# Optimization experiments

Measured on AMD Instinct MI355X. Metric: run time of the kernel, lower is better.

The kernel has to match this reference:

```python
import jax, jax.numpy as jnp
import numpy as np

EPS = 1e-5  # BatchNorm eps; eval mode with default running stats (mean=0, var=1)


def _bn(h, gamma, beta):
    # eval-mode BatchNorm2d with running_mean=0, running_var=1
    scale = gamma / jnp.sqrt(1.0 + EPS)
    return h * scale[None, :, None, None] + beta[None, :, None, None]


def _conv1x1(h, w, b):
    # 1x1 conv == channel matmul. h: [B,C,H,W], w: [O,C], b: [O]
    return jnp.einsum('bchw,oc->bohw', h, w) + b[None, :, None, None]


def setup_inputs() -> dict:
    key = jax.random.key(0)
    ks = jax.random.split(key, 16)
    B, C, H, W = 8, 64, 64, 64
    inp = {
        'x': jax.random.normal(ks[0], (B, C, H, W), dtype=jnp.float32),
        'saliency_map': jax.random.uniform(ks[1], (B, H, W), dtype=jnp.float32),
    }
    i = 2
    for name in ('q', 'k', 'v'):
        inp[f'w_{name}'] = jax.random.normal(ks[i], (C, C), dtype=jnp.float32) * (1.0 / np.sqrt(C)); i += 1
        inp[f'b_{name}'] = jax.random.normal(ks[i], (C,), dtype=jnp.float32) * 0.02; i += 1
        inp[f'g_{name}'] = 1.0 + 0.1 * jax.random.normal(ks[i], (C,), dtype=jnp.float32); i += 1
        inp[f'be_{name}'] = jax.random.normal(ks[i], (C,), dtype=jnp.float32) * 0.02; i += 1
    inp['g_o'] = 1.0 + 0.1 * jax.random.normal(ks[14], (C,), dtype=jnp.float32)
    inp['be_o'] = jax.random.normal(ks[15], (C,), dtype=jnp.float32) * 0.02
    return inp


def reference(x, saliency_map, w_q, b_q, g_q, be_q, w_k, b_k, g_k, be_k,
              w_v, b_v, g_v, be_v, g_o, be_o):
    B, C, H, W = x.shape
    HW = H * W
    query = _bn(_conv1x1(x, w_q, b_q), g_q, be_q).reshape(B, C, HW)
    key_ = _bn(_conv1x1(x, w_k, b_k), g_k, be_k).reshape(B, C, HW)
    value = _bn(_conv1x1(x, w_v, b_v), g_v, be_v).reshape(B, C, HW)
    mask = saliency_map.reshape(B, 1, HW)  # broadcast over channels == repeat
    query = query * mask
    # scores[b,i,j] = sum_c q[b,c,i] * k[b,c,j]; softmax over j (no scaling)
    scores = jnp.einsum('bci,bcj->bij', query, key_)
    attn = jax.nn.softmax(scores, axis=-1)
    # out[b,c,j] = sum_i v[b,c,i] * attn[b,i,j]
    enhanced = jnp.einsum('bci,bij->bcj', value, attn).reshape(B, C, H, W)
    enhanced = enhanced + x
    return _bn(enhanced, g_o, be_o)
```

## Files before the change

### kernel.cpp

```cpp
#include <hip/hip_runtime.h>

#define EPS 1e-5f

typedef __attribute__((ext_vector_type(8)))  short    s8b;
typedef __attribute__((ext_vector_type(16))) float    f32x16;
typedef __attribute__((ext_vector_type(4)))  float    f32x4;
typedef __attribute__((ext_vector_type(4)))  unsigned u32x4;

__device__ __forceinline__ unsigned cvt_pk_bf16(float lo, float hi) {
    unsigned r;
    asm("v_cvt_pk_bf16_f32 %0, %1, %2" : "=v"(r) : "v"(lo), "v"(hi));
    return r;
}
__device__ __forceinline__ void permswap(unsigned &a, unsigned &b) {
    asm("v_permlane32_swap_b32 %0, %1" : "+v"(a), "+v"(b));
}
union PackAB { u32x4 u; s8b s; };

__device__ __forceinline__ unsigned short f2bf(float f) {
    union { float f; unsigned u; } v; v.f = f;
    unsigned r = v.u + 0x7FFFu + ((v.u >> 16) & 1u);
    return (unsigned short)(r >> 16);
}


__global__ __launch_bounds__(256) void qkv_kernel(
    const float* __restrict__ x, const float* __restrict__ sal,
    const float* __restrict__ wq, const float* __restrict__ bq,
    const float* __restrict__ gq, const float* __restrict__ beq,
    const float* __restrict__ wk, const float* __restrict__ bk,
    const float* __restrict__ gk, const float* __restrict__ bek,
    const float* __restrict__ wv, const float* __restrict__ bv,
    const float* __restrict__ gv, const float* __restrict__ bev,
    short* __restrict__ Qf, short* __restrict__ Kf, short* __restrict__ Vf)
{
    __shared__ float w_lds[3][64][64];
    __shared__ float sc_lds[3][64];
    __shared__ float bb_lds[3][64];
    __shared__ float x_lds[64][68];
    __shared__ short v_lds[64 * 64];

    const int t = threadIdx.x;
    const int b = blockIdx.x & 7;
    const int p0 = (blockIdx.x >> 3) * 64;

    if (t < 192) {
        int m = t >> 6, o = t & 63;
        const float* g  = (m == 0) ? gq  : (m == 1) ? gk  : gv;
        const float* be = (m == 0) ? beq : (m == 1) ? bek : bev;
        const float* bi = (m == 0) ? bq  : (m == 1) ? bk  : bv;
        float s = g[o] * rsqrtf(1.0f + EPS);
        sc_lds[m][o] = s;
        bb_lds[m][o] = bi[o] * s + be[o];
    }
    __syncthreads();

    for (int rep = 0; rep < 12; ++rep) {
        int idx = (rep * 256 + t) * 4;
        int m = idx >> 12;
        int r = idx & 4095;
        int o = r >> 6;
        const float* w = (m == 0) ? wq : (m == 1) ? wk : wv;
        float4 v4 = *reinterpret_cast<const float4*>(w + r);
        float s = sc_lds[m][o];
        int c0 = r & 63;
        w_lds[m][o][c0 + 0] = v4.x * s;
        w_lds[m][o][c0 + 1] = v4.y * s;
        w_lds[m][o][c0 + 2] = v4.z * s;
        w_lds[m][o][c0 + 3] = v4.w * s;
    }
    for (int rep = 0; rep < 4; ++rep) {
        int idx = (rep * 256 + t) * 4;
        int c = idx >> 6, p = idx & 63;
        float4 v4 = *reinterpret_cast<const float4*>(
            x + (((size_t)(b * 64 + c)) << 12) + p0 + p);
        *reinterpret_cast<float4*>(&x_lds[c][p]) = v4;
    }
    __syncthreads();

    const int p = t & 63, og = t >> 6;
    const int i = p0 + p;
    float xr[64];
#pragma unroll
    for (int c = 0; c < 64; ++c) xr[c] = x_lds[c][p];
    const float mask = sal[(((size_t)b) << 12) + i];

#pragma unroll
    for (int m = 0; m < 3; ++m) {
        float outv[16];
#pragma unroll
        for (int oo = 0; oo < 16; ++oo) {
            int o = og * 16 + oo;
            float acc = bb_lds[m][o];
#pragma unroll
            for (int c = 0; c < 64; ++c) acc += w_lds[m][o][c] * xr[c];
            outv[oo] = acc;
        }
        if (m < 2) {
            if (m == 0) {
#pragma unroll
                for (int oo = 0; oo < 16; ++oo) outv[oo] *= mask;
            }
            short* dst = (m == 0) ? Qf : Kf;
            size_t base =
                ((((size_t)(b * 128 + (i >> 5)) * 4 + og) * 2) * 32 + (i & 31)) * 8;
            u32x4 pk0, pk1;
            pk0.x = cvt_pk_bf16(outv[0],  outv[1]);
            pk0.y = cvt_pk_bf16(outv[2],  outv[3]);
            pk0.z = cvt_pk_bf16(outv[4],  outv[5]);
            pk0.w = cvt_pk_bf16(outv[6],  outv[7]);
            pk1.x = cvt_pk_bf16(outv[8],  outv[9]);
            pk1.y = cvt_pk_bf16(outv[10], outv[11]);
            pk1.z = cvt_pk_bf16(outv[12], outv[13]);
            pk1.w = cvt_pk_bf16(outv[14], outv[15]);
            *reinterpret_cast<u32x4*>(dst + base)       = pk0;
            *reinterpret_cast<u32x4*>(dst + base + 256) = pk1;
        } else {
#pragma unroll
            for (int oo = 0; oo < 16; ++oo) {
                int c = og * 16 + oo;
                int sidx = (c * 64 + p) ^ ((c & 7) << 3);
                v_lds[sidx] = (short)f2bf(outv[oo]);
            }
        }
    }
    __syncthreads();

    const size_t vbase = (size_t)(b * 128 + (p0 >> 5)) * 2048;
#pragma unroll
    for (int r = 0; r < 2; ++r) {
        int f = r * 256 + t;
        int c = f & 63;
        int iL = ((f >> 6) & 7) * 8;
        int sidx = (c * 64 + iL) ^ ((c & 7) << 3);
        u32x4 val = *reinterpret_cast<const u32x4*>(&v_lds[sidx]);
        *reinterpret_cast<u32x4*>(Vf + vbase + (size_t)f * 8) = val;
    }
}

__global__ __launch_bounds__(256, 4) void rowsum_kernel(
    const short* __restrict__ Qf, const short* __restrict__ Kf,
    float* __restrict__ inv_l)
{
    __shared__ float part[4][32];

    const int t = threadIdx.x;
    const int b = blockIdx.x & 7;
    const int it = blockIdx.x >> 3;
    const int wave = t >> 6, lane = t & 63;
    const int l31 = lane & 31, hi = lane >> 5;

    const short* qp = Qf +
        ((((size_t)(b * 128 + it) * 4) * 2 + hi) * 32 + l31) * 8;
    s8b qf[4];
#pragma unroll
    for (int s = 0; s < 4; ++s)
        qf[s] = *reinterpret_cast<const s8b*>(qp + s * 512);

    float lsum[16];
#pragma unroll
    for (int r = 0; r < 16; ++r) lsum[r] = 0.f;

    for (int jb = wave; jb < 128; jb += 4) {
        const short* kp = Kf +
            ((((size_t)(b * 128 + jb) * 4) * 2 + hi) * 32 + l31) * 8;
        s8b kf[4];
#pragma unroll
        for (int s = 0; s < 4; ++s)
            kf[s] = *reinterpret_cast<const s8b*>(kp + s * 512);
        f32x16 sacc;
#pragma unroll
        for (int r = 0; r < 16; ++r) sacc[r] = 0.f;
#pragma unroll
        for (int s = 0; s < 4; ++s)
            sacc = __builtin_amdgcn_mfma_f32_32x32x16_bf16(qf[s], kf[s], sacc, 0, 0, 0);
#pragma unroll
        for (int r = 0; r < 16; ++r) lsum[r] += __expf(sacc[r]);
    }

#pragma unroll
    for (int off = 1; off < 32; off <<= 1)
#pragma unroll
        for (int r = 0; r < 16; ++r) lsum[r] += __shfl_xor(lsum[r], off);

    if (l31 == 0) {
#pragma unroll
        for (int r = 0; r < 16; ++r) {
            int iloc = (r & 3) + 8 * (r >> 2) + 4 * hi;
            part[wave][iloc] = lsum[r];
        }
    }
    __syncthreads();
    if (t < 32)
        inv_l[(((size_t)b) << 12) + it * 32 + t] =
            1.0f / (part[0][t] + part[1][t] + part[2][t] + part[3][t]);
}

__global__ __launch_bounds__(512, 4) void attnout_kernel(
    const short* __restrict__ Qf, const short* __restrict__ Kf,
    const short* __restrict__ Vf, const float* __restrict__ inv_l,
    const float* __restrict__ x, const float* __restrict__ go,
    const float* __restrict__ beo, float* __restrict__ out)
{
    __shared__ float red[2][3][64][33];

    const int t = threadIdx.x;
    const int b = blockIdx.x & 7;
    const int jt = blockIdx.x >> 3;
    const int wave = t >> 6, lane = t & 63;
    const int wr = wave >> 1;
    const int wc = wave & 1;
    const int l31 = lane & 31, hi = lane >> 5;

    const short* kp = Kf +
        ((((size_t)(b * 128 + jt * 2 + wc) * 4) * 2 + hi) * 32 + l31) * 8;
    s8b kf[4];
#pragma unroll
    for (int s = 0; s < 4; ++s)
        kf[s] = *reinterpret_cast<const s8b*>(kp + s * 512);

    f32x16 acc0, acc1;
#pragma unroll
    for (int r = 0; r < 16; ++r) { acc0[r] = 0.f; acc1[r] = 0.f; }

    const float* lip = inv_l + (((size_t)b) << 12);

    for (int ii = 0; ii < 32; ++ii) {
        const int ib = ii * 4 + wr;
        const short* qp = Qf +
            ((((size_t)(b * 128 + ib) * 4) * 2 + hi) * 32 + l31) * 8;
        s8b qf[4];
#pragma unroll
        for (int s = 0; s < 4; ++s)
            qf[s] = *reinterpret_cast<const s8b*>(qp + s * 512);

        const short* vp = Vf +
            ((((size_t)(b * 128 + ib) * 2) * 2 + hi) * 64 + l31) * 8;
        s8b vf[2][2];
#pragma unroll
        for (int s2 = 0; s2 < 2; ++s2)
#pragma unroll
            for (int nf = 0; nf < 2; ++nf)
                vf[s2][nf] = *reinterpret_cast<const s8b*>(
                    vp + s2 * 1024 + nf * 256);

        f32x4 li[4];
#pragma unroll
        for (int g = 0; g < 4; ++g)
            li[g] = *reinterpret_cast<const f32x4*>(lip + ib * 32 + 4 * hi + 8 * g);

        f32x16 sacc;
#pragma unroll
        for (int r = 0; r < 16; ++r) sacc[r] = 0.f;
#pragma unroll
        for (int s = 0; s < 4; ++s)
            sacc = __builtin_amdgcn_mfma_f32_32x32x16_bf16(qf[s], kf[s], sacc, 0, 0, 0);

        float p[16];
#pragma unroll
        for (int g = 0; g < 4; ++g)
#pragma unroll
            for (int q = 0; q < 4; ++q)
                p[g * 4 + q] = __expf(sacc[g * 4 + q]) * li[g][q];

        unsigned a0 = cvt_pk_bf16(p[0],  p[1]);
        unsigned a1 = cvt_pk_bf16(p[2],  p[3]);
        unsigned a2 = cvt_pk_bf16(p[4],  p[5]);
        unsigned a3 = cvt_pk_bf16(p[6],  p[7]);
        unsigned b0 = cvt_pk_bf16(p[8],  p[9]);
        unsigned b1 = cvt_pk_bf16(p[10], p[11]);
        unsigned b2 = cvt_pk_bf16(p[12], p[13]);
        unsigned b3 = cvt_pk_bf16(p[14], p[15]);
        permswap(a0, a2); permswap(a1, a3);
        permswap(b0, b2); permswap(b1, b3);
        PackAB pa0, pa1;
        pa0.u.x = a0; pa0.u.y = a1; pa0.u.z = a2; pa0.u.w = a3;
        pa1.u.x = b0; pa1.u.y = b1; pa1.u.z = b2; pa1.u.w = b3;

        acc0 = __builtin_amdgcn_mfma_f32_32x32x16_bf16(pa0.s, vf[0][0], acc0, 0, 0, 0);
        acc1 = __builtin_amdgcn_mfma_f32_32x32x16_bf16(pa0.s, vf[0][1], acc1, 0, 0, 0);
        acc0 = __builtin_amdgcn_mfma_f32_32x32x16_bf16(pa1.s, vf[1][0], acc0, 0, 0, 0);
        acc1 = __builtin_amdgcn_mfma_f32_32x32x16_bf16(pa1.s, vf[1][1], acc1, 0, 0, 0);
    }

    if (wr > 0) {
#pragma unroll
        for (int nf = 0; nf < 2; ++nf) {
            const f32x16& A = nf ? acc1 : acc0;
            int c = nf * 32 + l31;
#pragma unroll
            for (int g = 0; g < 4; ++g) {
                f32x4 v;
                v.x = A[g * 4 + 0]; v.y = A[g * 4 + 1];
                v.z = A[g * 4 + 2]; v.w = A[g * 4 + 3];
                *reinterpret_cast<f32x4*>(&red[wc][wr - 1][c][g * 8 + 4 * hi]) = v;
            }
        }
    }
    __syncthreads();
    if (wr == 0) {
#pragma unroll
        for (int nf = 0; nf < 2; ++nf) {
            const f32x16& A = nf ? acc1 : acc0;
            int c = nf * 32 + l31;
            const float sc = go[c] * rsqrtf(1.0f + EPS);
            const float bb = beo[c];
            size_t rowb = (((size_t)(b * 64 + c)) << 12) + jt * 64 + wc * 32;
#pragma unroll
            for (int g = 0; g < 4; ++g) {
                int jl = g * 8 + 4 * hi;
                f32x4 p0 = *reinterpret_cast<const f32x4*>(&red[wc][0][c][jl]);
                f32x4 p1 = *reinterpret_cast<const f32x4*>(&red[wc][1][c][jl]);
                f32x4 p2 = *reinterpret_cast<const f32x4*>(&red[wc][2][c][jl]);
                f32x4 xv = *reinterpret_cast<const f32x4*>(x + rowb + jl);
                f32x4 ov;
                ov.x = (A[g * 4 + 0] + p0.x + p1.x + p2.x + xv.x) * sc + bb;
                ov.y = (A[g * 4 + 1] + p0.y + p1.y + p2.y + xv.y) * sc + bb;
                ov.z = (A[g * 4 + 2] + p0.z + p1.z + p2.z + xv.z) * sc + bb;
                ov.w = (A[g * 4 + 3] + p0.w + p1.w + p2.w + xv.w) * sc + bb;
                *reinterpret_cast<f32x4*>(out + rowb + jl) = ov;
            }
        }
    }
}

extern "C" void kernel_launch(void* const* d_in, const int* in_sizes, int n_in,
                              void* d_out, int out_size, void* d_ws, size_t ws_size,
                              hipStream_t stream)
{
    (void)in_sizes; (void)n_in; (void)out_size; (void)ws_size;
    const float* x   = (const float*)d_in[0];
    const float* sal = (const float*)d_in[1];
    const float* wq  = (const float*)d_in[2];  const float* bq  = (const float*)d_in[3];
    const float* gq  = (const float*)d_in[4];  const float* beq = (const float*)d_in[5];
    const float* wk  = (const float*)d_in[6];  const float* bk  = (const float*)d_in[7];
    const float* gk  = (const float*)d_in[8];  const float* bek = (const float*)d_in[9];
    const float* wv  = (const float*)d_in[10]; const float* bv  = (const float*)d_in[11];
    const float* gv  = (const float*)d_in[12]; const float* bev = (const float*)d_in[13];
    const float* go  = (const float*)d_in[14]; const float* beo = (const float*)d_in[15];
    float* out = (float*)d_out;

    short* ws = (short*)d_ws;
    short* Qf = ws;
    short* Kf = ws + 2097152;
    short* Vf = ws + 4194304;
    float* il = (float*)(ws + 6291456);

    qkv_kernel<<<512, 256, 0, stream>>>(x, sal, wq, bq, gq, beq,
                                        wk, bk, gk, bek, wv, bv, gv, bev,
                                        Qf, Kf, Vf);
    rowsum_kernel<<<1024, 256, 0, stream>>>(Qf, Kf, il);
    attnout_kernel<<<512, 512, 0, stream>>>(Qf, Kf, Vf, il, x, go, beo, out);
}
```

Measured before the change: 188.9 us.

## Use MFMA for QKV projection, fold log2e into Q, software-pipeline attention loops

The QKV 1x1-conv projection moves from scalar FP32 FMAs to bf16 MFMA. Weights are split into hi/lo bf16 parts to keep accuracy, x is converted to bf16, and Q fragments are produced directly in MFMA-friendly packing. The softmax scale log2e is folded into the Q projection so the kernels can use exp2 instead of exp. The rowsum and attnout loops are double-buffered with K/Q/V prefetch and s_setprio around MFMA bursts. attnout is re-gridded to 1024 blocks of 256 threads, each handling one 32-column tile. This risks bf16 rounding of x in the projection and changes occupancy and reduction structure.

```diff
diff --git a/kernel.cpp b/kernel.cpp
--- a/kernel.cpp
+++ b/kernel.cpp
@@ -1,8 +1,10 @@
 #include <hip/hip_runtime.h>
 
 #define EPS 1e-5f
+#define LOG2E 1.4426950408889634f
 
 typedef __attribute__((ext_vector_type(8)))  short    s8b;
+typedef __attribute__((ext_vector_type(4)))  short    s4b;
 typedef __attribute__((ext_vector_type(16))) float    f32x16;
 typedef __attribute__((ext_vector_type(4)))  float    f32x4;
 typedef __attribute__((ext_vector_type(4)))  unsigned u32x4;
@@ -21,6 +23,10 @@
     union { float f; unsigned u; } v; v.f = f;
     unsigned r = v.u + 0x7FFFu + ((v.u >> 16) & 1u);
     return (unsigned short)(r >> 16);
+}
+__device__ __forceinline__ float bf2f(unsigned short h) {
+    union { unsigned u; float f; } v; v.u = ((unsigned)h) << 16;
+    return v.f;
 }
 
 
@@ -34,11 +40,11 @@
     const float* __restrict__ gv, const float* __restrict__ bev,
     short* __restrict__ Qf, short* __restrict__ Kf, short* __restrict__ Vf)
 {
-    __shared__ float w_lds[3][64][64];
+    __shared__ short wbf[6][4096];
+    __shared__ short xbf[4096];
+    __shared__ short v_lds[4096];
     __shared__ float sc_lds[3][64];
     __shared__ float bb_lds[3][64];
-    __shared__ float x_lds[64][68];
-    __shared__ short v_lds[64 * 64];
 
     const int t = threadIdx.x;
     const int b = blockIdx.x & 7;
@@ -49,9 +55,10 @@
         const float* g  = (m == 0) ? gq  : (m == 1) ? gk  : gv;
         const float* be = (m == 0) ? beq : (m == 1) ? bek : bev;
         const float* bi = (m == 0) ? bq  : (m == 1) ? bk  : bv;
-        float s = g[o] * rsqrtf(1.0f + EPS);
+        float lam = (m == 0) ? LOG2E : 1.0f;
+        float s = g[o] * rsqrtf(1.0f + EPS) * lam;
         sc_lds[m][o] = s;
-        bb_lds[m][o] = bi[o] * s + be[o];
+        bb_lds[m][o] = bi[o] * s + be[o] * lam;
     }
     __syncthreads();
 
@@ -59,68 +66,113 @@
         int idx = (rep * 256 + t) * 4;
         int m = idx >> 12;
         int r = idx & 4095;
-        int o = r >> 6;
+        int o = r >> 6, c0 = r & 63;
         const float* w = (m == 0) ? wq : (m == 1) ? wk : wv;
         float4 v4 = *reinterpret_cast<const float4*>(w + r);
         float s = sc_lds[m][o];
-        int c0 = r & 63;
-        w_lds[m][o][c0 + 0] = v4.x * s;
-        w_lds[m][o][c0 + 1] = v4.y * s;
-        w_lds[m][o][c0 + 2] = v4.z * s;
-        w_lds[m][o][c0 + 3] = v4.w * s;
-    }
-    for (int rep = 0; rep < 4; ++rep) {
-        int idx = (rep * 256 + t) * 4;
-        int c = idx >> 6, p = idx & 63;
-        float4 v4 = *reinterpret_cast<const float4*>(
-            x + (((size_t)(b * 64 + c)) << 12) + p0 + p);
-        *reinterpret_cast<float4*>(&x_lds[c][p]) = v4;
+        float w0 = v4.x * s, w1 = v4.y * s, w2 = v4.z * s, w3 = v4.w * s;
+        unsigned short h0 = f2bf(w0), h1 = f2bf(w1), h2 = f2bf(w2), h3 = f2bf(w3);
+        s4b hv, lv;
+        hv[0] = (short)h0; hv[1] = (short)h1; hv[2] = (short)h2; hv[3] = (short)h3;
+        lv[0] = (short)f2bf(w0 - bf2f(h0));
+        lv[1] = (short)f2bf(w1 - bf2f(h1));
+        lv[2] = (short)f2bf(w2 - bf2f(h2));
+        lv[3] = (short)f2bf(w3 - bf2f(h3));
+        int sidx = (o * 64 + c0) ^ ((o & 7) << 3);
+        *reinterpret_cast<s4b*>(&wbf[m * 2 + 0][sidx]) = hv;
+        *reinterpret_cast<s4b*>(&wbf[m * 2 + 1][sidx]) = lv;
+    }
+    {
+        const int xp = t & 63;
+        const int cgrp = (t >> 6) * 4;
+        const float* xb = x + ((size_t)(b * 64) << 12) + p0 + xp;
+        for (int rep = 0; rep < 4; ++rep) {
+            int cb = cgrp + rep * 16;
+            float x0 = xb[(size_t)(cb + 0) << 12];
+            float x1 = xb[(size_t)(cb + 1) << 12];
+            float x2 = xb[(size_t)(cb + 2) << 12];
+            float x3 = xb[(size_t)(cb + 3) << 12];
+            s4b pk;
+            pk[0] = (short)f2bf(x0); pk[1] = (short)f2bf(x1);
+            pk[2] = (short)f2bf(x2); pk[3] = (short)f2bf(x3);
+            int sidx = (xp * 64 + cb) ^ ((xp & 7) << 3);
+            *reinterpret_cast<s4b*>(&xbf[sidx]) = pk;
+        }
     }
     __syncthreads();
 
-    const int p = t & 63, og = t >> 6;
-    const int i = p0 + p;
-    float xr[64];
-#pragma unroll
-    for (int c = 0; c < 64; ++c) xr[c] = x_lds[c][p];
-    const float mask = sal[(((size_t)b) << 12) + i];
+    const int lane = t & 63, wave = t >> 6;
+    const int l31 = lane & 31, hi = lane >> 5;
+    const int phalf = wave & 1, ohalf = wave >> 1;
+    const int prow = phalf * 32 + l31;
+    const int orow = ohalf * 32 + l31;
+    const int ib = (p0 >> 5) + phalf;
+    const int swz = (l31 & 7) << 3;
+
+    s8b bx[4];
+#pragma unroll
+    for (int s = 0; s < 4; ++s)
+        bx[s] = *reinterpret_cast<const s8b*>(
+            &xbf[(prow * 64 + s * 16 + hi * 8) ^ ((prow & 7) << 3)]);
+
+    const float msk = sal[(((size_t)b) << 12) + p0 + prow];
 
 #pragma unroll
     for (int m = 0; m < 3; ++m) {
-        float outv[16];
-#pragma unroll
-        for (int oo = 0; oo < 16; ++oo) {
-            int o = og * 16 + oo;
-            float acc = bb_lds[m][o];
-#pragma unroll
-            for (int c = 0; c < 64; ++c) acc += w_lds[m][o][c] * xr[c];
-            outv[oo] = acc;
+        s8b ah[4], al[4];
+#pragma unroll
+        for (int s = 0; s < 4; ++s) {
+            int sidx = (orow * 64 + s * 16 + hi * 8) ^ swz;
+            ah[s] = *reinterpret_cast<const s8b*>(&wbf[m * 2 + 0][sidx]);
+            al[s] = *reinterpret_cast<const s8b*>(&wbf[m * 2 + 1][sidx]);
+        }
+        f32x16 d;
+#pragma unroll
+        for (int r = 0; r < 16; ++r) d[r] = 0.f;
+#pragma unroll
+        for (int s = 0; s < 4; ++s)
+            d = __builtin_amdgcn_mfma_f32_32x32x16_bf16(ah[s], bx[s], d, 0, 0, 0);
+#pragma unroll
+        for (int s = 0; s < 4; ++s)
+            d = __builtin_amdgcn_mfma_f32_32x32x16_bf16(al[s], bx[s], d, 0, 0, 0);
+
+        float pv[16];
+#pragma unroll
+        for (int g = 0; g < 4; ++g) {
+            f32x4 bb = *reinterpret_cast<const f32x4*>(
+                &bb_lds[m][ohalf * 32 + 8 * g + 4 * hi]);
+#pragma unroll
+            for (int q = 0; q < 4; ++q) pv[g * 4 + q] = d[g * 4 + q] + bb[q];
+        }
+        if (m == 0) {
+#pragma unroll
+            for (int r = 0; r < 16; ++r) pv[r] *= msk;
         }
         if (m < 2) {
-            if (m == 0) {
-#pragma unroll
-                for (int oo = 0; oo < 16; ++oo) outv[oo] *= mask;
-            }
+            unsigned a0 = cvt_pk_bf16(pv[0],  pv[1]);
+            unsigned a1 = cvt_pk_bf16(pv[2],  pv[3]);
+            unsigned a2 = cvt_pk_bf16(pv[4],  pv[5]);
+            unsigned a3 = cvt_pk_bf16(pv[6],  pv[7]);
+            unsigned b0 = cvt_pk_bf16(pv[8],  pv[9]);
+            unsigned b1 = cvt_pk_bf16(pv[10], pv[11]);
+            unsigned b2 = cvt_pk_bf16(pv[12], pv[13]);
+            unsigned b3 = cvt_pk_bf16(pv[14], pv[15]);
+            permswap(a0, a2); permswap(a1, a3);
+            permswap(b0, b2); permswap(b1, b3);
+            PackAB pa0, pa1;
+            pa0.u.x = a0; pa0.u.y = a1; pa0.u.z = a2; pa0.u.w = a3;
+            pa1.u.x = b0; pa1.u.y = b1; pa1.u.z = b2; pa1.u.w = b3;
             short* dst = (m == 0) ? Qf : Kf;
             size_t base =
-                ((((size_t)(b * 128 + (i >> 5)) * 4 + og) * 2) * 32 + (i & 31)) * 8;
-            u32x4 pk0, pk1;
-            pk0.x = cvt_pk_bf16(outv[0],  outv[1]);
-            pk0.y = cvt_pk_bf16(outv[2],  outv[3]);
-            pk0.z = cvt_pk_bf16(outv[4],  outv[5]);
-            pk0.w = cvt_pk_bf16(outv[6],  outv[7]);
-            pk1.x = cvt_pk_bf16(outv[8],  outv[9]);
-            pk1.y = cvt_pk_bf16(outv[10], outv[11]);
-            pk1.z = cvt_pk_bf16(outv[12], outv[13]);
-            pk1.w = cvt_pk_bf16(outv[14], outv[15]);
-            *reinterpret_cast<u32x4*>(dst + base)       = pk0;
-            *reinterpret_cast<u32x4*>(dst + base + 256) = pk1;
+                ((((size_t)(b * 128 + ib) * 4 + ohalf * 2) * 2 + hi) * 32 + l31) * 8;
+            *reinterpret_cast<u32x4*>(dst + base)       = pa0.u;
+            *reinterpret_cast<u32x4*>(dst + base + 512) = pa1.u;
         } else {
 #pragma unroll
-            for (int oo = 0; oo < 16; ++oo) {
-                int c = og * 16 + oo;
-                int sidx = (c * 64 + p) ^ ((c & 7) << 3);
-                v_lds[sidx] = (short)f2bf(outv[oo]);
+            for (int r = 0; r < 16; ++r) {
+                int c = ohalf * 32 + (r & 3) + 8 * (r >> 2) + 4 * hi;
+                int sidx = (c * 64 + prow) ^ ((c & 7) << 3);
+                v_lds[sidx] = (short)f2bf(pv[r]);
             }
         }
     }
@@ -138,6 +190,24 @@
     }
 }
 
+#define LOADK(JB, DST) {                                                      \
+    const short* _kp = Kf +                                                   \
+        ((((size_t)(b * 128 + (JB)) * 4) * 2 + hi) * 32 + l31) * 8;           \
+    DST[0] = *reinterpret_cast<const s8b*>(_kp);                              \
+    DST[1] = *reinterpret_cast<const s8b*>(_kp + 512);                        \
+    DST[2] = *reinterpret_cast<const s8b*>(_kp + 1024);                       \
+    DST[3] = *reinterpret_cast<const s8b*>(_kp + 1536); }
+
+#define RBODY(KARR) {                                                         \
+    f32x16 sacc;                                                              \
+    _Pragma("unroll") for (int r = 0; r < 16; ++r) sacc[r] = 0.f;             \
+    __builtin_amdgcn_s_setprio(1);                                            \
+    _Pragma("unroll") for (int s = 0; s < 4; ++s)                             \
+        sacc = __builtin_amdgcn_mfma_f32_32x32x16_bf16(qf[s], KARR[s], sacc, 0, 0, 0); \
+    __builtin_amdgcn_s_setprio(0);                                            \
+    _Pragma("unroll") for (int r = 0; r < 16; ++r)                            \
+        lsum[r] += __builtin_exp2f(sacc[r]); }
+
 __global__ __launch_bounds__(256, 4) void rowsum_kernel(
     const short* __restrict__ Qf, const short* __restrict__ Kf,
     float* __restrict__ inv_l)
@@ -161,21 +231,13 @@
 #pragma unroll
     for (int r = 0; r < 16; ++r) lsum[r] = 0.f;
 
-    for (int jb = wave; jb < 128; jb += 4) {
-        const short* kp = Kf +
-            ((((size_t)(b * 128 + jb) * 4) * 2 + hi) * 32 + l31) * 8;
-        s8b kf[4];
-#pragma unroll
-        for (int s = 0; s < 4; ++s)
-            kf[s] = *reinterpret_cast<const s8b*>(kp + s * 512);
-        f32x16 sacc;
-#pragma unroll
-        for (int r = 0; r < 16; ++r) sacc[r] = 0.f;
-#pragma unroll
-        for (int s = 0; s < 4; ++s)
-            sacc = __builtin_amdgcn_mfma_f32_32x32x16_bf16(qf[s], kf[s], sacc, 0, 0, 0);
-#pragma unroll
-        for (int r = 0; r < 16; ++r) lsum[r] += __expf(sacc[r]);
+    s8b kA[4], kB[4];
+    LOADK(wave, kA);
+    for (int ii = 0; ii < 32; ii += 2) {
+        LOADK(wave + (ii + 1) * 4, kB);
+        RBODY(kA);
+        if (ii + 2 < 32) { LOADK(wave + (ii + 2) * 4, kA); }
+        RBODY(kB);
     }
 
 #pragma unroll
@@ -196,24 +258,68 @@
             1.0f / (part[0][t] + part[1][t] + part[2][t] + part[3][t]);
 }
 
-__global__ __launch_bounds__(512, 4) void attnout_kernel(
+#define LOADQ(IB, DST) {                                                      \
+    const short* _qp = Qf +                                                   \
+        ((((size_t)(b * 128 + (IB)) * 4) * 2 + hi) * 32 + l31) * 8;           \
+    DST[0] = *reinterpret_cast<const s8b*>(_qp);                              \
+    DST[1] = *reinterpret_cast<const s8b*>(_qp + 512);                        \
+    DST[2] = *reinterpret_cast<const s8b*>(_qp + 1024);                       \
+    DST[3] = *reinterpret_cast<const s8b*>(_qp + 1536); }
+
+#define LOADV(IB) {                                                           \
+    const short* _vp = Vf +                                                   \
+        ((((size_t)(b * 128 + (IB)) * 2) * 2 + hi) * 64 + l31) * 8;           \
+    vf[0] = *reinterpret_cast<const s8b*>(_vp);                               \
+    vf[1] = *reinterpret_cast<const s8b*>(_vp + 256);                         \
+    vf[2] = *reinterpret_cast<const s8b*>(_vp + 1024);                        \
+    vf[3] = *reinterpret_cast<const s8b*>(_vp + 1280); }
+
+#define ABODY(QARR, IB) {                                                     \
+    f32x16 sacc;                                                              \
+    _Pragma("unroll") for (int r = 0; r < 16; ++r) sacc[r] = 0.f;             \
+    __builtin_amdgcn_s_setprio(1);                                            \
+    _Pragma("unroll") for (int s = 0; s < 4; ++s)                             \
+        sacc = __builtin_amdgcn_mfma_f32_32x32x16_bf16(QARR[s], kf[s], sacc, 0, 0, 0); \
+    __builtin_amdgcn_s_setprio(0);                                            \
+    float p[16];                                                              \
+    const int _ibase = (IB) * 32 + 4 * hi;                                    \
+    _Pragma("unroll") for (int g = 0; g < 4; ++g) {                           \
+        f32x4 li = *reinterpret_cast<const f32x4*>(lip + _ibase + 8 * g);     \
+        _Pragma("unroll") for (int q = 0; q < 4; ++q)                         \
+            p[g * 4 + q] = __builtin_exp2f(sacc[g * 4 + q]) * li[q];          \
+    }                                                                         \
+    unsigned a0 = cvt_pk_bf16(p[0],  p[1]),  a1 = cvt_pk_bf16(p[2],  p[3]);   \
+    unsigned a2 = cvt_pk_bf16(p[4],  p[5]),  a3 = cvt_pk_bf16(p[6],  p[7]);   \
+    unsigned b0 = cvt_pk_bf16(p[8],  p[9]),  b1 = cvt_pk_bf16(p[10], p[11]);  \
+    unsigned b2 = cvt_pk_bf16(p[12], p[13]), b3 = cvt_pk_bf16(p[14], p[15]);  \
+    permswap(a0, a2); permswap(a1, a3); permswap(b0, b2); permswap(b1, b3);   \
+    PackAB pa0, pa1;                                                          \
+    pa0.u.x = a0; pa0.u.y = a1; pa0.u.z = a2; pa0.u.w = a3;                   \
+    pa1.u.x = b0; pa1.u.y = b1; pa1.u.z = b2; pa1.u.w = b3;                   \
+    __builtin_amdgcn_s_setprio(1);                                            \
+    acc0 = __builtin_amdgcn_mfma_f32_32x32x16_bf16(pa0.s, vf[0], acc0, 0, 0, 0); \
+    acc1 = __builtin_amdgcn_mfma_f32_32x32x16_bf16(pa0.s, vf[1], acc1, 0, 0, 0); \
+    acc0 = __builtin_amdgcn_mfma_f32_32x32x16_bf16(pa1.s, vf[2], acc0, 0, 0, 0); \
+    acc1 = __builtin_amdgcn_mfma_f32_32x32x16_bf16(pa1.s, vf[3], acc1, 0, 0, 0); \
+    __builtin_amdgcn_s_setprio(0); }
+
+__global__ __launch_bounds__(256, 4) void attnout_kernel(
     const short* __restrict__ Qf, const short* __restrict__ Kf,
     const short* __restrict__ Vf, const float* __restrict__ inv_l,
     const float* __restrict__ x, const float* __restrict__ go,
     const float* __restrict__ beo, float* __restrict__ out)
 {
-    __shared__ float red[2][3][64][33];
+    __shared__ float red[3][64][33];
 
     const int t = threadIdx.x;
     const int b = blockIdx.x & 7;
-    const int jt = blockIdx.x >> 3;
+    const int jb = blockIdx.x >> 3;
     const int wave = t >> 6, lane = t & 63;
-    const int wr = wave >> 1;
-    const int wc = wave & 1;
+    const int wr = wave;
     const int l31 = lane & 31, hi = lane >> 5;
 
     const short* kp = Kf +
-        ((((size_t)(b * 128 + jt * 2 + wc) * 4) * 2 + hi) * 32 + l31) * 8;
+        ((((size_t)(b * 128 + jb) * 4) * 2 + hi) * 32 + l31) * 8;
     s8b kf[4];
 #pragma unroll
     for (int s = 0; s < 4; ++s)
@@ -225,62 +331,18 @@
 
     const float* lip = inv_l + (((size_t)b) << 12);
 
-    for (int ii = 0; ii < 32; ++ii) {
-        const int ib = ii * 4 + wr;
-        const short* qp = Qf +
-            ((((size_t)(b * 128 + ib) * 4) * 2 + hi) * 32 + l31) * 8;
-        s8b qf[4];
-#pragma unroll
-        for (int s = 0; s < 4; ++s)
-            qf[s] = *reinterpret_cast<const s8b*>(qp + s * 512);
-
-        const short* vp = Vf +
-            ((((size_t)(b * 128 + ib) * 2) * 2 + hi) * 64 + l31) * 8;
-        s8b vf[2][2];
-#pragma unroll
-        for (int s2 = 0; s2 < 2; ++s2)
-#pragma unroll
-            for (int nf = 0; nf < 2; ++nf)
-                vf[s2][nf] = *reinterpret_cast<const s8b*>(
-                    vp + s2 * 1024 + nf * 256);
-
-        f32x4 li[4];
-#pragma unroll
-        for (int g = 0; g < 4; ++g)
-            li[g] = *reinterpret_cast<const f32x4*>(lip + ib * 32 + 4 * hi + 8 * g);
-
-        f32x16 sacc;
-#pragma unroll
-        for (int r = 0; r < 16; ++r) sacc[r] = 0.f;
-#pragma unroll
-        for (int s = 0; s < 4; ++s)
-            sacc = __builtin_amdgcn_mfma_f32_32x32x16_bf16(qf[s], kf[s], sacc, 0, 0, 0);
-
-        float p[16];
-#pragma unroll
-        for (int g = 0; g < 4; ++g)
-#pragma unroll
-            for (int q = 0; q < 4; ++q)
-                p[g * 4 + q] = __expf(sacc[g * 4 + q]) * li[g][q];
-
-        unsigned a0 = cvt_pk_bf16(p[0],  p[1]);
-        unsigned a1 = cvt_pk_bf16(p[2],  p[3]);
-        unsigned a2 = cvt_pk_bf16(p[4],  p[5]);
-        unsigned a3 = cvt_pk_bf16(p[6],  p[7]);
-        unsigned b0 = cvt_pk_bf16(p[8],  p[9]);
-        unsigned b1 = cvt_pk_bf16(p[10], p[11]);
-        unsigned b2 = cvt_pk_bf16(p[12], p[13]);
-        unsigned b3 = cvt_pk_bf16(p[14], p[15]);
-        permswap(a0, a2); permswap(a1, a3);
-        permswap(b0, b2); permswap(b1, b3);
-        PackAB pa0, pa1;
-        pa0.u.x = a0; pa0.u.y = a1; pa0.u.z = a2; pa0.u.w = a3;
-        pa1.u.x = b0; pa1.u.y = b1; pa1.u.z = b2; pa1.u.w = b3;
-
-        acc0 = __builtin_amdgcn_mfma_f32_32x32x16_bf16(pa0.s, vf[0][0], acc0, 0, 0, 0);
-        acc1 = __builtin_amdgcn_mfma_f32_32x32x16_bf16(pa0.s, vf[0][1], acc1, 0, 0, 0);
-        acc0 = __builtin_amdgcn_mfma_f32_32x32x16_bf16(pa1.s, vf[1][0], acc0, 0, 0, 0);
-        acc1 = __builtin_amdgcn_mfma_f32_32x32x16_bf16(pa1.s, vf[1][1], acc1, 0, 0, 0);
+    s8b qA[4], qB[4], vf[4];
+    LOADQ(wr, qA);
+    LOADV(wr);
+    for (int ii = 0; ii < 32; ii += 2) {
+        const int ibA = ii * 4 + wr;
+        const int ibB = ibA + 4;
+        LOADQ(ibB, qB);
+        ABODY(qA, ibA);
+        LOADV(ibB);
+        if (ii + 2 < 32) { LOADQ(ibA + 8, qA); }
+        ABODY(qB, ibB);
+        if (ii + 2 < 32) { LOADV(ibA + 8); }
     }
 
     if (wr > 0) {
@@ -293,7 +355,7 @@
                 f32x4 v;
                 v.x = A[g * 4 + 0]; v.y = A[g * 4 + 1];
                 v.z = A[g * 4 + 2]; v.w = A[g * 4 + 3];
-                *reinterpret_cast<f32x4*>(&red[wc][wr - 1][c][g * 8 + 4 * hi]) = v;
+                *reinterpret_cast<f32x4*>(&red[wr - 1][c][g * 8 + 4 * hi]) = v;
             }
         }
     }
@@ -305,13 +367,13 @@
             int c = nf * 32 + l31;
             const float sc = go[c] * rsqrtf(1.0f + EPS);
             const float bb = beo[c];
-            size_t rowb = (((size_t)(b * 64 + c)) << 12) + jt * 64 + wc * 32;
+            size_t rowb = (((size_t)(b * 64 + c)) << 12) + jb * 32;
 #pragma unroll
             for (int g = 0; g < 4; ++g) {
                 int jl = g * 8 + 4 * hi;
-                f32x4 p0 = *reinterpret_cast<const f32x4*>(&red[wc][0][c][jl]);
-                f32x4 p1 = *reinterpret_cast<const f32x4*>(&red[wc][1][c][jl]);
-                f32x4 p2 = *reinterpret_cast<const f32x4*>(&red[wc][2][c][jl]);
+                f32x4 p0 = *reinterpret_cast<const f32x4*>(&red[0][c][jl]);
+                f32x4 p1 = *reinterpret_cast<const f32x4*>(&red[1][c][jl]);
+                f32x4 p2 = *reinterpret_cast<const f32x4*>(&red[2][c][jl]);
                 f32x4 xv = *reinterpret_cast<const f32x4*>(x + rowb + jl);
                 f32x4 ov;
                 ov.x = (A[g * 4 + 0] + p0.x + p1.x + p2.x + xv.x) * sc + bb;
@@ -350,5 +412,5 @@
                                         wk, bk, gk, bek, wv, bv, gv, bev,
                                         Qf, Kf, Vf);
     rowsum_kernel<<<1024, 256, 0, stream>>>(Qf, Kf, il);
-    attnout_kernel<<<512, 512, 0, stream>>>(Qf, Kf, Vf, il, x, go, beo, out);
-}
+    attnout_kernel<<<1024, 256, 0, stream>>>(Qf, Kf, Vf, il, x, go, beo, out);
+}
```

Measured after the change: 222.6 us. 1.18x slower.
